# Kernel tuning notes

Hardware: AMD Instinct MI355X
Metric: run time of the kernel (lower is better)

## Reference

```python
import jax, jax.numpy as jnp
import numpy as np

B, T, D = 2, 2048, 2048
H = 8
DK = 256   # head_qk_dim
DV = 512   # head_v_dim
C = 64     # retention chunk size
EPS = 1e-5
ROPE_BASE = 10000.0


def _rotary(x):
    # x: [B, T, H, DK], non-interleaved (rotate-half) rotary over full head dim
    half = DK // 2
    inv_freq = 1.0 / (ROPE_BASE ** (jnp.arange(0, DK, 2, dtype=jnp.float32) / DK))
    freqs = jnp.arange(T, dtype=jnp.float32)[:, None] * inv_freq[None, :]  # [T, half]
    cos = jnp.cos(freqs)[None, :, None, :].astype(x.dtype)
    sin = jnp.sin(freqs)[None, :, None, :].astype(x.dtype)
    x1, x2 = x[..., :half], x[..., half:]
    return jnp.concatenate([x1 * cos - x2 * sin, x2 * cos + x1 * sin], axis=-1)


def setup_inputs() -> dict:
    key = jax.random.key(0)
    ks = jax.random.split(key, 6)
    s = 2.0 ** (-2.5) * (2.0 / 2048.0) ** 0.5  # xavier_uniform-ish scale, gain 2^-2.5
    return {
        "hidden_states": jax.random.normal(ks[0], (B, T, D), jnp.float32),
        "Wq": jax.random.normal(ks[1], (H * DK, D), jnp.float32) * s,
        "Wk": jax.random.normal(ks[2], (H * DK, D), jnp.float32) * s,
        "Wv": jax.random.normal(ks[3], (H * DV, D), jnp.float32) * s,
        "Wg": jax.random.normal(ks[4], (H * DV, D), jnp.float32) * s,
        "Wo": jax.random.normal(ks[5], (D, H * DV), jnp.float32) * s,
        "g_norm_weight": jnp.ones((DV,), jnp.float32),
    }


def reference(hidden_states, Wq, Wk, Wv, Wg, Wo, g_norm_weight):
    x = hidden_states  # [B, T, D]
    q = (x @ Wq.T).reshape(B, T, H, DK)
    k = (x @ Wk.T).reshape(B, T, H, DK)
    q = _rotary(q)
    k = _rotary(k)
    q = q.transpose(0, 2, 1, 3) * (DK ** -0.5)        # [B, H, T, DK]
    k = k.transpose(0, 2, 1, 3)                       # [B, H, T, DK]
    v = (x @ Wv.T).reshape(B, T, H, DV).transpose(0, 2, 1, 3)  # [B, H, T, DV]

    # RetNet multi-scale per-head decay
    logb = jnp.log(1.0 - 2.0 ** (-5.0 - jnp.arange(H, dtype=jnp.float32)))  # [H]
    i = jnp.arange(C, dtype=jnp.float32)
    # intra-chunk decay mask b^{i-j} for i>=j: [H, C, C]
    Dmask = jnp.where(i[:, None] >= i[None, :],
                      jnp.exp(logb[:, None, None] * (i[:, None] - i[None, :])), 0.0)
    q_dec = jnp.exp(logb[:, None] * (i + 1.0))        # [H, C]  decay applied to q vs carried state
    k_dec = jnp.exp(logb[:, None] * (C - 1.0 - i))    # [H, C]  decay applied to k for state update
    chunk_dec = jnp.exp(logb * C)                     # [H]

    N = T // C
    qc = q.reshape(B, H, N, C, DK).transpose(2, 0, 1, 3, 4)  # [N, B, H, C, DK]
    kc = k.reshape(B, H, N, C, DK).transpose(2, 0, 1, 3, 4)
    vc = v.reshape(B, H, N, C, DV).transpose(2, 0, 1, 3, 4)

    def body(S, inp):
        qi, ki, vi = inp  # [B,H,C,DK], [B,H,C,DK], [B,H,C,DV]
        inter = jnp.einsum('bhcd,bhdv->bhcv', qi * q_dec[None, :, :, None], S)
        scores = jnp.einsum('bhcd,bhmd->bhcm', qi, ki) * Dmask[None]
        o = inter + jnp.einsum('bhcm,bhmv->bhcv', scores, vi)
        S_new = S * chunk_dec[None, :, None, None] + \
                jnp.einsum('bhcd,bhcv->bhdv', ki * k_dec[None, :, :, None], vi)
        return S_new, o

    S0 = jnp.zeros((B, H, DK, DV), x.dtype)
    _, oc = jax.lax.scan(body, S0, (qc, kc, vc))  # oc: [N, B, H, C, DV]
    o = oc.transpose(1, 2, 0, 3, 4).reshape(B, H, T, DV).transpose(0, 2, 1, 3)  # [B, T, H, DV]

    g = (x @ Wg.T).reshape(B, T, H, DV)
    # fused RMSNorm + swish gate (per head_v_dim)
    o_n = o * jax.lax.rsqrt(jnp.mean(o * o, axis=-1, keepdims=True) + EPS) * g_norm_weight
    o = o_n * (g * jax.nn.sigmoid(g))
    return o.reshape(B, T, H * DV) @ Wo.T  # [B, T, D]
```

## Files before the change

### kernel.cpp

```cpp
#include <hip/hip_runtime.h>


typedef unsigned short u16;
typedef unsigned int u32;
typedef short bf16x8 __attribute__((ext_vector_type(8)));
typedef short s16x4 __attribute__((ext_vector_type(4)));
typedef float f32x4 __attribute__((ext_vector_type(4)));
typedef u32 u32x2 __attribute__((ext_vector_type(2)));
typedef u32 u32x4 __attribute__((ext_vector_type(4)));

typedef __attribute__((address_space(3))) u32 lds_u32;
typedef __attribute__((address_space(1))) const u32 gbl_u32;

__device__ __forceinline__ float bf2f(u16 u) {
    union { u32 i; float f; } x; x.i = ((u32)u) << 16; return x.f;
}
__device__ __forceinline__ u16 f2bf(float f) {
    union { float f; u32 i; } x; x.f = f;
    u32 u = x.i;
    u += 0x7fffu + ((u >> 16) & 1u);
    return (u16)(u >> 16);
}
__device__ __forceinline__ f32x4 mfma16(bf16x8 a, bf16x8 b, f32x4 c) {
    return __builtin_amdgcn_mfma_f32_16x16x32_bf16(a, b, c, 0, 0, 0);
}
__device__ __forceinline__ void gload16(const u16* g, u16* lds) {
    __builtin_amdgcn_global_load_lds((gbl_u32*)(unsigned long long)g,
                                     (lds_u32*)(u32)(unsigned long long)lds, 16, 0, 0);
}

__global__ __launch_bounds__(256)
void cvt_bf16(const float* __restrict__ src, u16* __restrict__ dst)
{
    size_t i = ((size_t)blockIdx.x * 256 + threadIdx.x) * 8;
    f32x4 a = *(const f32x4*)(src + i);
    f32x4 b = *(const f32x4*)(src + i + 4);
    bf16x8 r;
#pragma unroll
    for (int j = 0; j < 4; j++) { r[j] = (short)f2bf(a[j]); r[j + 4] = (short)f2bf(b[j]); }
    *(bf16x8*)(dst + i) = r;
}

template<bool CF32>
__global__ __launch_bounds__(256, 2)
void gemm_bt(const u16* __restrict__ A, const u16* __restrict__ Bm,
             void* __restrict__ Cv, int N, int K)
{
    __shared__ u16 Ab[128 * 64];
    __shared__ u16 Bb[128 * 64];
    const int tid = threadIdx.x;
    const int lane = tid & 63, wave = tid >> 6;
    const int quad = lane >> 4, l16 = lane & 15;
    const int tn = blockIdx.x, tm = blockIdx.y;
    const int wr = wave >> 1, wc = wave & 1;

    f32x4 acc[4][4];
#pragma unroll
    for (int i = 0; i < 4; i++)
#pragma unroll
        for (int j = 0; j < 4; j++) acc[i][j] = (f32x4){0.f, 0.f, 0.f, 0.f};

    const u16* Abase = A + (size_t)tm * 128 * K;
    const u16* Bbase = Bm + (size_t)tn * 128 * K;
    const int rsub = lane >> 3, csub = (lane & 7) * 8;

    for (int k0 = 0; k0 < K; k0 += 64) {
        __syncthreads();
#pragma unroll
        for (int i = 0; i < 4; i++) {
            int chunk = wave * 4 + i;
            int r = chunk * 8 + rsub;
            gload16(Abase + (size_t)r * K + k0 + csub, Ab + chunk * 512);
            gload16(Bbase + (size_t)r * K + k0 + csub, Bb + chunk * 512);
        }
        __syncthreads();
#pragma unroll
        for (int kc = 0; kc < 2; kc++) {
            bf16x8 af[4], bfr[4];
#pragma unroll
            for (int mt = 0; mt < 4; mt++)
                af[mt] = *(const bf16x8*)(Ab + (wr * 64 + mt * 16 + l16) * 64 + kc * 32 + quad * 8);
#pragma unroll
            for (int nt = 0; nt < 4; nt++)
                bfr[nt] = *(const bf16x8*)(Bb + (wc * 64 + nt * 16 + l16) * 64 + kc * 32 + quad * 8);
#pragma unroll
            for (int mt = 0; mt < 4; mt++)
#pragma unroll
                for (int nt = 0; nt < 4; nt++)
                    acc[mt][nt] = mfma16(af[mt], bfr[nt], acc[mt][nt]);
        }
    }
    const int row0 = tm * 128 + wr * 64 + quad * 4;
    const int col0 = tn * 128 + wc * 64 + l16;
#pragma unroll
    for (int mt = 0; mt < 4; mt++)
#pragma unroll
        for (int nt = 0; nt < 4; nt++)
#pragma unroll
            for (int r = 0; r < 4; r++) {
                size_t idx = (size_t)(row0 + mt * 16 + r) * N + col0 + nt * 16;
                if constexpr (CF32) ((float*)Cv)[idx] = acc[mt][nt][r];
                else                ((u16*)Cv)[idx]   = f2bf(acc[mt][nt][r]);
            }
}

__global__ __launch_bounds__(256, 2)
void rotary_scores(u16* __restrict__ q, const u16* __restrict__ k,
                   u16* __restrict__ kT, u16* __restrict__ P)
{
    __shared__ u16 qS[64 * 264];
    __shared__ u16 kS[64 * 264];
    const int tid = threadIdx.x;
    const int lane = tid & 63, wave = tid >> 6;
    const int quad = lane >> 4, l16 = lane & 15;
    const int bx = blockIdx.x;
    const int bh = bx & 15, n = bx >> 4;
    const int b = bh >> 3, h = bh & 7;
    const int t0 = n * 64;

    const int row = tid >> 2;
    const int j0 = (tid & 3) * 32;
    const size_t rowbase = (size_t)(b * 2048 + t0 + row) * 2048 + h * 256;
    const float tpos = (float)(t0 + row);
#pragma unroll
    for (int i = 0; i < 4; i++) {
        int j = j0 + i * 8;
        bf16x8 x1 = *(const bf16x8*)(q + rowbase + j);
        bf16x8 x2 = *(const bf16x8*)(q + rowbase + j + 128);
        bf16x8 y1 = *(const bf16x8*)(k + rowbase + j);
        bf16x8 y2 = *(const bf16x8*)(k + rowbase + j + 128);
        bf16x8 o1, o2, p1, p2;
#pragma unroll
        for (int e = 0; e < 8; e++) {
            float inv = expf((-9.210340371976184f / 128.f) * (float)(j + e));
            float ang = tpos * inv;
            float sv = sinf(ang), cv = cosf(ang);
            float a = bf2f((u16)x1[e]), bb = bf2f((u16)x2[e]);
            o1[e] = (short)f2bf((a * cv - bb * sv) * 0.0625f);
            o2[e] = (short)f2bf((bb * cv + a * sv) * 0.0625f);
            float e1 = bf2f((u16)y1[e]), e2 = bf2f((u16)y2[e]);
            p1[e] = (short)f2bf(e1 * cv - e2 * sv);
            p2[e] = (short)f2bf(e2 * cv + e1 * sv);
        }
        *(bf16x8*)(q + rowbase + j)       = o1;
        *(bf16x8*)(q + rowbase + j + 128) = o2;
        *(bf16x8*)(qS + row * 264 + j)       = o1;
        *(bf16x8*)(qS + row * 264 + j + 128) = o2;
        *(bf16x8*)(kS + row * 264 + j)       = p1;
        *(bf16x8*)(kS + row * 264 + j + 128) = p2;
    }
    __syncthreads();

    const float logb = logf(1.0f - exp2f(-5.0f - (float)h));
    f32x4 sc[4];
#pragma unroll
    for (int i = 0; i < 4; i++) sc[i] = (f32x4){0.f, 0.f, 0.f, 0.f};
#pragma unroll
    for (int kc = 0; kc < 8; kc++) {
        bf16x8 af = *(const bf16x8*)(qS + (wave * 16 + l16) * 264 + kc * 32 + quad * 8);
#pragma unroll
        for (int mt = 0; mt < 4; mt++) {
            bf16x8 bk = *(const bf16x8*)(kS + (mt * 16 + l16) * 264 + kc * 32 + quad * 8);
            sc[mt] = mfma16(af, bk, sc[mt]);
        }
    }
    u16* Pb = P + ((size_t)(bh * 32 + n)) * 64 * 64;
#pragma unroll
    for (int r = 0; r < 4; r++) {
        int cr = wave * 16 + quad * 4 + r;
        float rowe = __expf(logb * (float)(cr - 63));
#pragma unroll
        for (int mt = 0; mt < 4; mt++) {
            int m = mt * 16 + l16;
            float val = (cr >= m) ? sc[mt][r] * rowe : 0.0f;
            Pb[cr * 64 + m] = f2bf(val);
        }
    }

    const int d = tid;
    u16* dst = kT + ((size_t)(bh * 256 + d)) * 2048 + t0;
#pragma unroll
    for (int g8 = 0; g8 < 8; g8++) {
        bf16x8 w;
#pragma unroll
        for (int e = 0; e < 8; e++) w[e] = (short)kS[(g8 * 8 + e) * 264 + d];
        *(bf16x8*)(dst + g8 * 8) = w;
    }
}

__global__ __launch_bounds__(512, 2)
void retention(const u16* __restrict__ Q, const u16* __restrict__ KT,
               const u16* __restrict__ V, const u16* __restrict__ P,
               u16* __restrict__ O)
{
    __shared__ u16 St[32 * 264];
    __shared__ u16 vsT[32 * 72];

    const int tid = threadIdx.x;
    const int lane = tid & 63, wave = tid >> 6;
    const int quad = lane >> 4, l16 = lane & 15;
    const int bx = blockIdx.x;
    const int bh = bx & 15, vt = bx >> 4;
    const int b = bh >> 3, h = bh & 7;
    const int cgrp = wave >> 1, vhalf = wave & 1;

    const float logb = logf(1.0f - exp2f(-5.0f - (float)h));
    const float cdec = __expf(logb * 64.0f);

    int cr[4];
    float qdecr[4];
#pragma unroll
    for (int r = 0; r < 4; r++) {
        cr[r] = cgrp * 16 + quad * 4 + r;
        qdecr[r] = __expf(logb * (float)(cr[r] + 1));
    }
    const int mv = tid >> 3;
    const int vc4 = (tid & 7) * 4;
    const float kdv = __expf(logb * (float)(63 - mv));

    for (int i = tid; i < 32 * 264; i += 512) St[i] = 0;

    f32x4 Sacc[2][2];
#pragma unroll
    for (int dt = 0; dt < 2; dt++)
#pragma unroll
        for (int nt = 0; nt < 2; nt++) Sacc[dt][nt] = (f32x4){0.f, 0.f, 0.f, 0.f};

    for (int n = 0; n < 32; n++) {
        const int t0 = n * 64;
        u32x2 vv = *(const u32x2*)(V + (size_t)(b * 2048 + t0 + mv) * 4096 + h * 512 + vt * 32 + vc4);
        bf16x8 qf[8];
#pragma unroll
        for (int kc = 0; kc < 8; kc++)
            qf[kc] = *(const bf16x8*)(Q + (size_t)(b * 2048 + t0 + cgrp * 16 + l16) * 2048
                                      + h * 256 + kc * 32 + quad * 8);
        bf16x8 ktf[2][2];
#pragma unroll
        for (int dt = 0; dt < 2; dt++)
#pragma unroll
            for (int kc2 = 0; kc2 < 2; kc2++)
                ktf[dt][kc2] = *(const bf16x8*)(KT + (size_t)(bh * 256 + wave * 32 + dt * 16 + l16) * 2048
                                                + t0 + kc2 * 32 + quad * 8);
        bf16x8 pf[2];
#pragma unroll
        for (int kc2 = 0; kc2 < 2; kc2++)
            pf[kc2] = *(const bf16x8*)(P + ((size_t)(bh * 32 + n) * 64 + cgrp * 16 + l16) * 64
                                       + kc2 * 32 + quad * 8);

        __syncthreads();

        {
            u16 e0 = (u16)(vv[0] & 0xffff), e1 = (u16)(vv[0] >> 16);
            u16 e2 = (u16)(vv[1] & 0xffff), e3 = (u16)(vv[1] >> 16);
            vsT[(vc4 + 0) * 72 + mv] = f2bf(bf2f(e0) * kdv);
            vsT[(vc4 + 1) * 72 + mv] = f2bf(bf2f(e1) * kdv);
            vsT[(vc4 + 2) * 72 + mv] = f2bf(bf2f(e2) * kdv);
            vsT[(vc4 + 3) * 72 + mv] = f2bf(bf2f(e3) * kdv);
        }
        f32x4 oacc = (f32x4){0.f, 0.f, 0.f, 0.f};
#pragma unroll
        for (int kc = 0; kc < 8; kc++) {
            bf16x8 bs = *(const bf16x8*)(St + (vhalf * 16 + l16) * 264 + kc * 32 + quad * 8);
            oacc = mfma16(qf[kc], bs, oacc);
        }

        __syncthreads();

#pragma unroll
        for (int dt = 0; dt < 2; dt++)
#pragma unroll
            for (int nt = 0; nt < 2; nt++)
#pragma unroll
                for (int e = 0; e < 4; e++) Sacc[dt][nt][e] *= cdec;
#pragma unroll
        for (int kc2 = 0; kc2 < 2; kc2++) {
            bf16x8 bv0 = *(const bf16x8*)(vsT + l16 * 72 + kc2 * 32 + quad * 8);
            bf16x8 bv1 = *(const bf16x8*)(vsT + (16 + l16) * 72 + kc2 * 32 + quad * 8);
#pragma unroll
            for (int dt = 0; dt < 2; dt++) {
                Sacc[dt][0] = mfma16(ktf[dt][kc2], bv0, Sacc[dt][0]);
                Sacc[dt][1] = mfma16(ktf[dt][kc2], bv1, Sacc[dt][1]);
            }
        }
#pragma unroll
        for (int r = 0; r < 4; r++) oacc[r] *= qdecr[r];
#pragma unroll
        for (int kc2 = 0; kc2 < 2; kc2++) {
            bf16x8 bv = *(const bf16x8*)(vsT + (vhalf * 16 + l16) * 72 + kc2 * 32 + quad * 8);
            oacc = mfma16(pf[kc2], bv, oacc);
        }
#pragma unroll
        for (int r = 0; r < 4; r++)
            O[(size_t)(b * 2048 + t0 + cr[r]) * 4096 + h * 512 + vt * 32 + vhalf * 16 + l16] =
                f2bf(oacc[r]);
#pragma unroll
        for (int dt = 0; dt < 2; dt++)
#pragma unroll
            for (int nt = 0; nt < 2; nt++) {
                s16x4 w;
#pragma unroll
                for (int r = 0; r < 4; r++) w[r] = (short)f2bf(Sacc[dt][nt][r]);
                *(s16x4*)(St + (nt * 16 + l16) * 264 + wave * 32 + dt * 16 + quad * 4) = w;
            }
    }
}

__global__ __launch_bounds__(256)
void norm_gate(const u16* __restrict__ O, const u16* __restrict__ G,
               const float* __restrict__ gw, u16* __restrict__ ON)
{
    const int lane = threadIdx.x & 63;
    const size_t row = (size_t)blockIdx.x * 4 + (threadIdx.x >> 6);
    bf16x8 ov = *(const bf16x8*)(O + row * 512 + lane * 8);
    bf16x8 gv = *(const bf16x8*)(G + row * 512 + lane * 8);
    f32x4 w0 = *(const f32x4*)(gw + lane * 8);
    f32x4 w1 = *(const f32x4*)(gw + lane * 8 + 4);
    float of[8], gf[8];
    float ss = 0.f;
#pragma unroll
    for (int j = 0; j < 8; j++) {
        of[j] = bf2f((u16)ov[j]);
        gf[j] = bf2f((u16)gv[j]);
        ss += of[j] * of[j];
    }
#pragma unroll
    for (int off = 32; off > 0; off >>= 1) ss += __shfl_down(ss, off);
    ss = __shfl(ss, 0);
    const float rms = rsqrtf(ss * (1.0f / 512.0f) + 1e-5f);
    bf16x8 res;
#pragma unroll
    for (int j = 0; j < 8; j++) {
        float wj = (j < 4) ? w0[j] : w1[j - 4];
        float xn = of[j] * rms * wj;
        float sg = gf[j] / (1.f + __expf(-gf[j]));
        res[j] = (short)f2bf(xn * sg);
    }
    *(bf16x8*)(ON + row * 512 + lane * 8) = res;
}

extern "C" void kernel_launch(void* const* d_in, const int* in_sizes, int n_in,
                              void* d_out, int out_size, void* d_ws, size_t ws_size,
                              hipStream_t stream)
{
    const float* x  = (const float*)d_in[0];
    const float* Wq = (const float*)d_in[1];
    const float* Wk = (const float*)d_in[2];
    const float* Wv = (const float*)d_in[3];
    const float* Wg = (const float*)d_in[4];
    const float* Wo = (const float*)d_in[5];
    const float* gw = (const float*)d_in[6];
    float* out = (float*)d_out;

    const size_t M8 = (size_t)4096 * 2048;
    u16* Pb = (u16*)d_ws;
    u16* q  = Pb + (size_t)16 * 32 * 64 * 64;
    u16* k  = q + M8;
    u16* kT = k + M8;
    u16* v  = kT + M8;
    u16* o  = v + 2 * M8;
    u16* xb = o + 2 * M8;
    u16* g  = q;
    u16* on = v;
    u16* wt = kT;

    dim3 blk(256, 1, 1), blk512(512, 1, 1);
    cvt_bf16<<<dim3(4096, 1, 1), blk, 0, stream>>>(x, xb);

    cvt_bf16<<<dim3(2048, 1, 1), blk, 0, stream>>>(Wq, wt);
    gemm_bt<false><<<dim3(16, 32, 1), blk, 0, stream>>>(xb, wt, q, 2048, 2048);
    cvt_bf16<<<dim3(2048, 1, 1), blk, 0, stream>>>(Wk, wt);
    gemm_bt<false><<<dim3(16, 32, 1), blk, 0, stream>>>(xb, wt, k, 2048, 2048);
    cvt_bf16<<<dim3(4096, 1, 1), blk, 0, stream>>>(Wv, wt);
    gemm_bt<false><<<dim3(32, 32, 1), blk, 0, stream>>>(xb, wt, v, 4096, 2048);

    rotary_scores<<<dim3(512, 1, 1), blk, 0, stream>>>(q, k, kT, Pb);
    retention<<<dim3(256, 1, 1), blk512, 0, stream>>>(q, kT, v, Pb, o);

    cvt_bf16<<<dim3(4096, 1, 1), blk, 0, stream>>>(Wg, kT);
    gemm_bt<false><<<dim3(32, 32, 1), blk, 0, stream>>>(xb, kT, g, 4096, 2048);
    norm_gate<<<dim3(8192, 1, 1), blk, 0, stream>>>(o, g, gw, on);
    cvt_bf16<<<dim3(4096, 1, 1), blk, 0, stream>>>(Wo, kT);
    gemm_bt<true><<<dim3(16, 32, 1), blk, 0, stream>>>(on, kT, out, 2048, 4096);
}
```

Measured before the change: 706.3 us.

## Add pipelined 256x256 GEMM and fuse Q/K projections into one launch

Adds a 512-thread GEMM kernel with 256x256 output tiles, double-buffered LDS staged through direct global-to-LDS loads, barrier-interleaved MFMA phases and priority hints. It replaces the 128-tile GEMM for the V and G projections. Wq and Wk are converted into one contiguous weight buffer so Q and K come from a single N=4096 GEMM, and the rotary and retention kernels now read with a 4096 row stride. The larger tiles are meant to raise operand reuse and overlap memory loads with matrix math, at the cost of heavy register use, a smaller grid of 256 blocks, and fragile hand-written waitcnt sequencing.

```diff
diff --git a/kernel.cpp b/kernel.cpp
--- a/kernel.cpp
+++ b/kernel.cpp
@@ -102,6 +102,122 @@
                 if constexpr (CF32) ((float*)Cv)[idx] = acc[mt][nt][r];
                 else                ((u16*)Cv)[idx]   = f2bf(acc[mt][nt][r]);
             }
+}
+
+__global__ __launch_bounds__(512, 2)
+void gemm256(const u16* __restrict__ A, const u16* __restrict__ Bm,
+             u16* __restrict__ C, int N, int K)
+{
+    __shared__ __align__(16) u16 As[2][2][256 * 32];
+    __shared__ __align__(16) u16 Bs[2][2][256 * 32];
+    const int tid = threadIdx.x;
+    const int lane = tid & 63, wave = tid >> 6;
+    const int quad = lane >> 4, l16 = lane & 15;
+    const int wm = wave >> 2, wn = wave & 3;
+    const int tn = blockIdx.x, tm = blockIdx.y;
+    const int NTm1 = K / 64 - 1;
+    const u16* Abase = A + (size_t)tm * 256 * K;
+    const u16* Bbase = Bm + (size_t)tn * 256 * K;
+    const int gr = tid >> 2;
+    const int gc = (tid & 3) * 8;
+    const int wv64 = wave * 64;
+
+    f32x4 acc[8][4];
+#pragma unroll
+    for (int i = 0; i < 8; i++)
+#pragma unroll
+        for (int j = 0; j < 4; j++) acc[i][j] = (f32x4){0.f, 0.f, 0.f, 0.f};
+
+    bf16x8 bq[8];
+    bf16x8 af[4];
+
+#define STAGE(arr, bf, kc, Gb, kt) do {                                         \
+    int kt_ = (kt); kt_ = (kt_ > NTm1) ? NTm1 : kt_;                            \
+    const u16* s_ = (Gb) + (size_t)gr * K + (size_t)kt_ * 64 + (kc) * 32 + gc;  \
+    gload16(s_,                 &arr[bf][kc][wv64 * 8]);                        \
+    gload16(s_ + (size_t)128 * K, &arr[bf][kc][(512 + wv64) * 8]);              \
+} while (0)
+
+#define LDA(bf, kc, mg) do {                                                    \
+    _Pragma("unroll")                                                           \
+    for (int j = 0; j < 4; j++)                                                 \
+        af[j] = *(const bf16x8*)&As[bf][kc][(wm * 128 + (mg) * 64 + j * 16 + l16) * 32 + quad * 8]; \
+} while (0)
+
+#define LDB(bf) do {                                                            \
+    _Pragma("unroll")                                                           \
+    for (int kc_ = 0; kc_ < 2; kc_++)                                           \
+        _Pragma("unroll")                                                       \
+        for (int n_ = 0; n_ < 4; n_++)                                          \
+            bq[kc_ * 4 + n_] = *(const bf16x8*)&Bs[bf][kc_][(wn * 64 + n_ * 16 + l16) * 32 + quad * 8]; \
+} while (0)
+
+#define MM16(kc, mg) do {                                                       \
+    _Pragma("unroll")                                                           \
+    for (int j = 0; j < 4; j++)                                                 \
+        _Pragma("unroll")                                                       \
+        for (int n_ = 0; n_ < 4; n_++)                                          \
+            acc[(mg) * 4 + j][n_] = mfma16(af[j], bq[(kc) * 4 + n_], acc[(mg) * 4 + j][n_]); \
+} while (0)
+
+#define BAR   __builtin_amdgcn_s_barrier()
+#define LGKM0 asm volatile("s_waitcnt lgkmcnt(0)" ::: "memory")
+#define VM6   asm volatile("s_waitcnt vmcnt(6)" ::: "memory")
+#define PRIO1 __builtin_amdgcn_s_setprio(1)
+#define PRIO0 __builtin_amdgcn_s_setprio(0)
+
+    STAGE(Bs, 0, 0, Bbase, 0);
+    STAGE(Bs, 0, 1, Bbase, 0);
+    STAGE(As, 0, 0, Abase, 0);
+    STAGE(As, 0, 1, Abase, 0);
+    asm volatile("s_waitcnt vmcnt(4)" ::: "memory");
+    STAGE(Bs, 1, 0, Bbase, 1);
+    STAGE(Bs, 1, 1, Bbase, 1);
+    STAGE(As, 1, 0, Abase, 1);
+    asm volatile("s_waitcnt vmcnt(6)" ::: "memory");
+    BAR;
+
+    const int NI = K / 128;
+    for (int it = 0; it < NI; ++it) {
+        const int t0 = 2 * it;
+        LDB(0); LDA(0, 0, 0); STAGE(As, 1, 1, Abase, t0 + 1);
+        BAR; LGKM0; PRIO1; MM16(0, 0); PRIO0; BAR;
+        LDA(0, 0, 1); STAGE(Bs, 0, 0, Bbase, t0 + 2);
+        BAR; LGKM0; PRIO1; MM16(0, 1); PRIO0; BAR;
+        LDA(0, 1, 0); STAGE(Bs, 0, 1, Bbase, t0 + 2);
+        BAR; LGKM0; PRIO1; MM16(1, 0); PRIO0; BAR;
+        LDA(0, 1, 1); STAGE(As, 0, 0, Abase, t0 + 2);
+        BAR; LGKM0; PRIO1; MM16(1, 1); PRIO0; VM6; BAR;
+        LDB(1); LDA(1, 0, 0); STAGE(As, 0, 1, Abase, t0 + 2);
+        BAR; LGKM0; PRIO1; MM16(0, 0); PRIO0; BAR;
+        LDA(1, 0, 1); STAGE(Bs, 1, 0, Bbase, t0 + 3);
+        BAR; LGKM0; PRIO1; MM16(0, 1); PRIO0; BAR;
+        LDA(1, 1, 0); STAGE(Bs, 1, 1, Bbase, t0 + 3);
+        BAR; LGKM0; PRIO1; MM16(1, 0); PRIO0; BAR;
+        LDA(1, 1, 1); STAGE(As, 1, 0, Abase, t0 + 3);
+        BAR; LGKM0; PRIO1; MM16(1, 1); PRIO0; VM6; BAR;
+    }
+    asm volatile("s_waitcnt vmcnt(0)" ::: "memory");
+
+    const int row0 = tm * 256 + wm * 128 + quad * 4;
+    const int col0 = tn * 256 + wn * 64 + l16;
+#pragma unroll
+    for (int mt = 0; mt < 8; mt++)
+#pragma unroll
+        for (int nt = 0; nt < 4; nt++)
+#pragma unroll
+            for (int r = 0; r < 4; r++)
+                C[(size_t)(row0 + mt * 16 + r) * N + col0 + nt * 16] = f2bf(acc[mt][nt][r]);
+
+#undef STAGE
+#undef LDA
+#undef LDB
+#undef MM16
+#undef BAR
+#undef LGKM0
+#undef VM6
+#undef PRIO1
+#undef PRIO0
 }
 
 __global__ __launch_bounds__(256, 2)
@@ -120,7 +236,7 @@
 
     const int row = tid >> 2;
     const int j0 = (tid & 3) * 32;
-    const size_t rowbase = (size_t)(b * 2048 + t0 + row) * 2048 + h * 256;
+    const size_t rowbase = (size_t)(b * 2048 + t0 + row) * 4096 + h * 256;
     const float tpos = (float)(t0 + row);
 #pragma unroll
     for (int i = 0; i < 4; i++) {
@@ -232,7 +348,7 @@
         bf16x8 qf[8];
 #pragma unroll
         for (int kc = 0; kc < 8; kc++)
-            qf[kc] = *(const bf16x8*)(Q + (size_t)(b * 2048 + t0 + cgrp * 16 + l16) * 2048
+            qf[kc] = *(const bf16x8*)(Q + (size_t)(b * 2048 + t0 + cgrp * 16 + l16) * 4096
                                       + h * 256 + kc * 32 + quad * 8);
         bf16x8 ktf[2][2];
 #pragma unroll
@@ -353,13 +469,12 @@
 
     const size_t M8 = (size_t)4096 * 2048;
     u16* Pb = (u16*)d_ws;
-    u16* q  = Pb + (size_t)16 * 32 * 64 * 64;
-    u16* k  = q + M8;
-    u16* kT = k + M8;
+    u16* qk = Pb + (size_t)16 * 32 * 64 * 64;
+    u16* kT = qk + 2 * M8;
     u16* v  = kT + M8;
     u16* o  = v + 2 * M8;
     u16* xb = o + 2 * M8;
-    u16* g  = q;
+    u16* g  = qk;
     u16* on = v;
     u16* wt = kT;
 
@@ -367,17 +482,16 @@
     cvt_bf16<<<dim3(4096, 1, 1), blk, 0, stream>>>(x, xb);
 
     cvt_bf16<<<dim3(2048, 1, 1), blk, 0, stream>>>(Wq, wt);
-    gemm_bt<false><<<dim3(16, 32, 1), blk, 0, stream>>>(xb, wt, q, 2048, 2048);
-    cvt_bf16<<<dim3(2048, 1, 1), blk, 0, stream>>>(Wk, wt);
-    gemm_bt<false><<<dim3(16, 32, 1), blk, 0, stream>>>(xb, wt, k, 2048, 2048);
+    cvt_bf16<<<dim3(2048, 1, 1), blk, 0, stream>>>(Wk, wt + (size_t)2048 * 2048);
+    gemm256<<<dim3(16, 16, 1), blk512, 0, stream>>>(xb, wt, qk, 4096, 2048);
     cvt_bf16<<<dim3(4096, 1, 1), blk, 0, stream>>>(Wv, wt);
-    gemm_bt<false><<<dim3(32, 32, 1), blk, 0, stream>>>(xb, wt, v, 4096, 2048);
-
-    rotary_scores<<<dim3(512, 1, 1), blk, 0, stream>>>(q, k, kT, Pb);
-    retention<<<dim3(256, 1, 1), blk512, 0, stream>>>(q, kT, v, Pb, o);
+    gemm256<<<dim3(16, 16, 1), blk512, 0, stream>>>(xb, wt, v, 4096, 2048);
+
+    rotary_scores<<<dim3(512, 1, 1), blk, 0, stream>>>(qk, qk + 2048, kT, Pb);
+    retention<<<dim3(256, 1, 1), blk512, 0, stream>>>(qk, kT, v, Pb, o);
 
     cvt_bf16<<<dim3(4096, 1, 1), blk, 0, stream>>>(Wg, kT);
-    gemm_bt<false><<<dim3(32, 32, 1), blk, 0, stream>>>(xb, kT, g, 4096, 2048);
+    gemm256<<<dim3(16, 16, 1), blk512, 0, stream>>>(xb, kT, g, 4096, 2048);
     norm_gate<<<dim3(8192, 1, 1), blk, 0, stream>>>(o, g, gw, on);
     cvt_bf16<<<dim3(4096, 1, 1), blk, 0, stream>>>(Wo, kT);
     gemm_bt<true><<<dim3(16, 32, 1), blk, 0, stream>>>(on, kT, out, 2048, 4096);
```

Measured after the change: 621.1 us. -12.1%, faster.
